# Performance work log

Hardware: AMD Instinct MI355X
Metric: run time of the kernel (lower is better)

## Reference

```python
import jax, jax.numpy as jnp
import numpy as np

B, S, D, H, FB, K, FC = 16, 512, 256, 8, 128, 64, 32


def setup_inputs() -> dict:
    key = jax.random.key(0)
    ks = jax.random.split(key, 16)
    g = lambda i, shp: jax.random.normal(ks[i], shp, dtype=jnp.float32)
    inp = {
        "B_target": g(0, (B, S, FB)),
        "B_infected": g(1, (B, S, FB)),
        "E_target": g(2, (B, S, D)),
        "E_infected": g(3, (B, S, D)),
        "C_target": jax.random.uniform(ks[4], (B, S, K, FC), dtype=jnp.float32),
        "C_infected": jax.random.uniform(ks[5], (B, S, K, FC), dtype=jnp.float32),
        # learned parameters
        "W_bs": g(6, (FB, 1)) * 0.1,
        "W_cs": g(7, (FC, 1)) * 0.1,
        "W1": g(8, (H, D, D)) * (1.0 / np.sqrt(D)),  # per-head Attn W1, batched
        "W2": g(9, (H, D, D)) * (1.0 / np.sqrt(D)),
        "gamma_bs": jnp.ones((S,), jnp.float32),
        "beta_bs": jnp.zeros((S,), jnp.float32),
        "gamma_cs": jnp.ones((S,), jnp.float32),
        "beta_cs": jnp.zeros((S,), jnp.float32),
        "W_f": g(10, (2, 1)) * 0.1,
    }
    return inp


def _weighted_sum(x, W):
    # tf.nn.softmax over trailing size-1 axis of [F,1] -> all ones (faithful)
    return jnp.squeeze(x @ jax.nn.softmax(W, axis=-1), -1)


def _l2norm(x):
    return x * jax.lax.rsqrt(jnp.maximum(jnp.sum(x * x, -1, keepdims=True), 1e-12))


def _layernorm(x, gamma, beta, eps=1e-16):
    m = jnp.mean(x, -1, keepdims=True)
    v = jnp.mean(jnp.square(x - m), -1, keepdims=True)
    return (x - m) * jax.lax.rsqrt(v + eps) * gamma + beta


def _kld(y_true, y_pred, eps=1e-7):
    yt = jnp.clip(y_true, eps, 1.0)
    yp = jnp.clip(y_pred, eps, 1.0)
    return jnp.sum(yt * jnp.log(yt / yp), -1)


def _attn_br(Bvec, E, W1, W2):
    # batched multi-head version of the per-head Attn loop
    Q = jnp.einsum('bsd,hde->bhse', E, W1)
    Kh = jnp.einsum('bsd,hde->bhse', E, W2)
    scale = 1.0 / jnp.sqrt(jnp.asarray(E.shape[-1], E.dtype))
    scores = jnp.einsum('bhse,bhte->bhst', Q, Kh) * scale  # [b,H,S,S]
    A = jax.nn.softmax(scores, axis=2)  # original softmax(axis=1) on [b,S,S]
    # Dot(axes=(1,1)) of [b,S] with [b,S,S] -> [b,S]; stack heads, transpose -> [b,S,H]
    return jnp.einsum('bs,bhst->bth', Bvec, A)


def reference(B_target, B_infected, E_target, E_infected, C_target, C_infected,
              W_bs, W_cs, W1, W2, gamma_bs, beta_bs, gamma_cs, beta_cs, W_f):
    Bt = _weighted_sum(B_target, W_bs)   # [b,S]
    Bi = _weighted_sum(B_infected, W_bs)
    BR_t = _attn_br(Bt, E_target, W1, W2)    # [b,S,H]
    BR_i = _attn_br(Bi, E_infected, W1, W2)
    # keras CosineSimilarity loss = -cos_sim
    cos = -jnp.sum(_l2norm(BR_i) * _l2norm(BR_t), -1)  # [b,S]
    BS_out = _layernorm(cos, gamma_bs, beta_bs)
    Ct = _weighted_sum(C_target, W_cs)   # [b,S,K]
    Ci = _weighted_sum(C_infected, W_cs)
    Cm = 0.5 * (Ct + Ci)
    Cv = 0.5 * _kld(Ci, Cm) + 0.5 * _kld(Ct, Cm)  # [b,S]
    CS_out = _layernorm(Cv, gamma_cs, beta_cs)
    composite = jnp.stack([BS_out, CS_out], axis=-1)  # [b,S,2]
    out = jnp.squeeze(composite @ jax.nn.softmax(W_f, axis=-1), -1)
    return (out, BS_out, CS_out)
```

## Files before the change

### kernel.cpp

```cpp
#include <hip/hip_runtime.h>

#define NB 16
#define NS 512
#define ND 256
#define NH 8
#define NFB 128
#define NK 64
#define NFC 32

using f16 = _Float16;
using f16x4 = __attribute__((ext_vector_type(4))) f16;
using f16x8 = __attribute__((ext_vector_type(8))) f16;
using f32x4 = __attribute__((ext_vector_type(4))) float;

__device__ inline float waveReduceSum(float v) {
    #pragma unroll
    for (int off = 32; off; off >>= 1) v += __shfl_down(v, off);
    return v;
}

__device__ inline f32x4 mfma16(f16x8 a, f16x8 b, f32x4 c) {
    return __builtin_amdgcn_mfma_f32_16x16x32_f16(a, b, c, 0, 0, 0);
}

__global__ __launch_bounds__(256) void k_prep(const float* __restrict__ W1, const float* __restrict__ W2,
                                              f16* __restrict__ Mth,
                                              const float* __restrict__ Et_in, const float* __restrict__ Ei_in,
                                              f16* __restrict__ Ot, f16* __restrict__ Oi,
                                              const float* __restrict__ Bt_in, const float* __restrict__ Bi_in,
                                              float* __restrict__ Bt, float* __restrict__ Bi,
                                              const float* __restrict__ Ct, const float* __restrict__ Ci,
                                              float* __restrict__ Cv) {
    __shared__ float Wa[64][36];
    __shared__ float Wb[64][36];
    int bid = blockIdx.x;
    int tid = threadIdx.x;

    if (bid < 128) {
        int h  = bid >> 4;
        int j0 = ((bid >> 2) & 3) * 64;
        int i0 = (bid & 3) * 64;
        const float* A  = W2 + (size_t)h * ND * ND;
        const float* Bm = W1 + (size_t)h * ND * ND;
        int r = tid >> 4, c = tid & 15;
        float acc[4][4] = {};
        for (int d0 = 0; d0 < ND; d0 += 32) {
            __syncthreads();
            #pragma unroll
            for (int i = 0; i < 2; ++i) {
                int sid = tid + i * 256;
                int row = sid >> 3, seg = sid & 7;
                *(float4*)&Wa[row][seg * 4] = *(const float4*)&A [(size_t)(j0 + row) * ND + d0 + seg * 4];
                *(float4*)&Wb[row][seg * 4] = *(const float4*)&Bm[(size_t)(i0 + row) * ND + d0 + seg * 4];
            }
            __syncthreads();
            #pragma unroll 8
            for (int d = 0; d < 32; ++d) {
                float a0 = Wa[r*4+0][d], a1 = Wa[r*4+1][d], a2 = Wa[r*4+2][d], a3 = Wa[r*4+3][d];
                float b0 = Wb[c*4+0][d], b1 = Wb[c*4+1][d], b2 = Wb[c*4+2][d], b3 = Wb[c*4+3][d];
                acc[0][0] += a0*b0; acc[0][1] += a0*b1; acc[0][2] += a0*b2; acc[0][3] += a0*b3;
                acc[1][0] += a1*b0; acc[1][1] += a1*b1; acc[1][2] += a1*b2; acc[1][3] += a1*b3;
                acc[2][0] += a2*b0; acc[2][1] += a2*b1; acc[2][2] += a2*b2; acc[2][3] += a2*b3;
                acc[3][0] += a3*b0; acc[3][1] += a3*b1; acc[3][2] += a3*b2; acc[3][3] += a3*b3;
            }
        }
        #pragma unroll
        for (int a = 0; a < 4; ++a)
            #pragma unroll
            for (int bb = 0; bb < 4; ++bb)
                Mth[(size_t)h * ND * ND + (size_t)(j0 + r * 4 + a) * ND + (i0 + c * 4 + bb)] = (f16)acc[a][bb];
    } else if (bid < 128 + 4096) {
        const int n4 = NB * NS * ND / 4;
        int i = (bid - 128) * 256 + tid;
        const float* src; f16* dst;
        if (i < n4) { src = Et_in; dst = Ot; }
        else        { src = Ei_in; dst = Oi; i -= n4; }
        float4 v = ((const float4*)src)[i];
        f16x4 o = { (f16)v.x, (f16)v.y, (f16)v.z, (f16)v.w };
        ((f16x4*)dst)[i] = o;
    } else if (bid < 128 + 8192) {
        int wid = ((bid - 128 - 4096) * 256 + tid) >> 6;
        int lane = tid & 63;
        const float* src; float* dst; int row;
        if (wid < NB * NS) { src = Bt_in; dst = Bt; row = wid; }
        else               { src = Bi_in; dst = Bi; row = wid - NB * NS; }
        float2 v = ((const float2*)(src + (size_t)row * NFB))[lane];
        float s = waveReduceSum(v.x + v.y);
        if (lane == 0) dst[row] = s;
    } else {
        int gw = ((bid - 128 - 8192) * 256 + tid) >> 6;
        int lane = tid & 63;
        const float* pt = Ct + ((size_t)gw * NK + lane) * NFC;
        const float* pi = Ci + ((size_t)gw * NK + lane) * NFC;
        float st = 0.f, si = 0.f;
        #pragma unroll
        for (int j = 0; j < NFC; j += 4) {
            float4 vt = *(const float4*)(pt + j); st += vt.x + vt.y + vt.z + vt.w;
            float4 vi = *(const float4*)(pi + j); si += vi.x + vi.y + vi.z + vi.w;
        }
        float cm = 0.5f * (st + si);
        float yp = fminf(fmaxf(cm, 1e-7f), 1.0f);
        float y1 = fminf(fmaxf(si, 1e-7f), 1.0f);
        float y2 = fminf(fmaxf(st, 1e-7f), 1.0f);
        float term = 0.5f * (y1 * logf(y1 / yp) + y2 * logf(y2 / yp));
        term = waveReduceSum(term);
        if (lane == 0) Cv[gw] = term;
    }
}

__global__ __launch_bounds__(256, 4) void k_attn4(const f16* __restrict__ Eft, const f16* __restrict__ Efi,
                                                  const f16* __restrict__ Mth,
                                                  const float* __restrict__ Bst, const float* __restrict__ Bsi,
                                                  float* __restrict__ PEt, float* __restrict__ PBt,
                                                  float* __restrict__ PEi, float* __restrict__ PBi) {
    int x = blockIdx.x;
    const f16* E; const float* Bvg; float *PE, *PB;
    if (x < 512) { E = Eft; Bvg = Bst; PE = PEt; PB = PBt; }
    else         { x -= 512; E = Efi; Bvg = Bsi; PE = PEi; PB = PBi; }
    int b = x >> 5, h = (x >> 2) & 7;
    int sc = x & 3;
    int s0 = sc * 128;
    const f16* Ebase = E + (size_t)b * NS * ND;
    const f16* Mh = Mth + (size_t)h * ND * ND;
    float* PEo = PE + (size_t)((b * NH + h) * 4 + sc) * NS;
    float* PBo = PB + (size_t)((b * NH + h) * 4 + sc) * NS;

    __shared__ f16 smem[2 * 32 * 264];
    __shared__ float pe_s[NS], pb_s[NS];

    int tid = threadIdx.x;
    int lane = tid & 63, w = tid >> 6;
    int l16 = lane & 15, ch = lane >> 4;

    pe_s[tid] = 0.f; pe_s[tid + 256] = 0.f;
    pb_s[tid] = 0.f; pb_s[tid + 256] = 0.f;

    int sw0 = s0 + w * 32;

    f16x8 ebf[2][8];
    #pragma unroll
    for (int st = 0; st < 2; ++st)
        #pragma unroll
        for (int ki = 0; ki < 8; ++ki)
            ebf[st][ki] = *(const f16x8*)&Ebase[(size_t)(sw0 + st * 16 + l16) * ND + ki * 32 + ch * 8];

    float bvr[2][4];
    #pragma unroll
    for (int st = 0; st < 2; ++st)
        #pragma unroll
        for (int r = 0; r < 4; ++r)
            bvr[st][r] = Bvg[b * NS + sw0 + st * 16 + 4 * ch + r];

    f16x8 af[2][8];
    #pragma unroll
    for (int jc = 0; jc < 8; ++jc) {
        __syncthreads();
        #pragma unroll
        for (int it = 0; it < 4; ++it) {
            int sid = tid + it * 256;
            int row = sid >> 5, seg = sid & 31;
            *(int4*)&smem[row * 264 + seg * 8] = *(const int4*)&Mh[(size_t)(jc * 32 + row) * ND + seg * 8];
        }
        __syncthreads();
        f32x4 acc[2][2] = {};
        #pragma unroll
        for (int ki = 0; ki < 8; ++ki) {
            f16x8 a0 = *(const f16x8*)&smem[(l16)      * 264 + ki * 32 + ch * 8];
            f16x8 a1 = *(const f16x8*)&smem[(16 + l16) * 264 + ki * 32 + ch * 8];
            acc[0][0] = mfma16(a0, ebf[0][ki], acc[0][0]);
            acc[0][1] = mfma16(a0, ebf[1][ki], acc[0][1]);
            acc[1][0] = mfma16(a1, ebf[0][ki], acc[1][0]);
            acc[1][1] = mfma16(a1, ebf[1][ki], acc[1][1]);
        }
        #pragma unroll
        for (int st = 0; st < 2; ++st) {
            f16x8 v;
            #pragma unroll
            for (int r = 0; r < 4; ++r) { v[r] = (f16)acc[0][st][r]; v[4 + r] = (f16)acc[1][st][r]; }
            af[st][jc] = v;
        }
    }
    __syncthreads();

    int4 v[4];
    #pragma unroll
    for (int i = 0; i < 4; ++i) {
        int sid = tid + i * 256;
        int row = sid >> 5, seg = sid & 31;
        v[i] = *(const int4*)&Ebase[(size_t)row * ND + seg * 8];
    }
    #pragma unroll
    for (int i = 0; i < 4; ++i) {
        int sid = tid + i * 256;
        int row = sid >> 5, seg = sid & 31;
        *(int4*)&smem[row * 264 + seg * 8] = v[i];
    }

    for (int t = 0; t < 16; ++t) {
        f16* cur = smem + (t & 1) * (32 * 264);
        f16* nxt = smem + ((t + 1) & 1) * (32 * 264);
        if (t < 15) {
            int t0n = (t + 1) * 32;
            #pragma unroll
            for (int i = 0; i < 4; ++i) {
                int sid = tid + i * 256;
                int row = sid >> 5, seg = sid & 31;
                v[i] = *(const int4*)&Ebase[(size_t)(t0n + row) * ND + seg * 8];
            }
        }
        __syncthreads();
        int t0 = t * 32;
        f32x4 sacc[2][2] = {};
        #pragma unroll
        for (int kk = 0; kk < 8; ++kk)
            #pragma unroll
            for (int nt = 0; nt < 2; ++nt) {
                const f16* ep = &cur[(nt * 16 + l16) * 264 + kk * 32 + 4 * ch];
                f16x4 lo = *(const f16x4*)ep;
                f16x4 hi = *(const f16x4*)(ep + 16);
                f16x8 bf = { lo[0], lo[1], lo[2], lo[3], hi[0], hi[1], hi[2], hi[3] };
                sacc[0][nt] = mfma16(af[0][kk], bf, sacc[0][nt]);
                sacc[1][nt] = mfma16(af[1][kk], bf, sacc[1][nt]);
            }
        if (t < 15) {
            #pragma unroll
            for (int i = 0; i < 4; ++i) {
                int sid = tid + i * 256;
                int row = sid >> 5, seg = sid & 31;
                *(int4*)&nxt[row * 264 + seg * 8] = v[i];
            }
        }
        #pragma unroll
        for (int nt = 0; nt < 2; ++nt) {
            float se = 0.f, sw = 0.f;
            #pragma unroll
            for (int st = 0; st < 2; ++st)
                #pragma unroll
                for (int r = 0; r < 4; ++r) {
                    float e = __expf(sacc[st][nt][r] * 0.0625f);
                    se += e; sw += bvr[st][r] * e;
                }
            se += __shfl_down(se, 32); se += __shfl_down(se, 16);
            sw += __shfl_down(sw, 32); sw += __shfl_down(sw, 16);
            if (ch == 0) {
                atomicAdd(&pe_s[t0 + nt * 16 + l16], se);
                atomicAdd(&pb_s[t0 + nt * 16 + l16], sw);
            }
        }
    }
    __syncthreads();
    PEo[tid]       = pe_s[tid];
    PEo[tid + 256] = pe_s[tid + 256];
    PBo[tid]       = pb_s[tid];
    PBo[tid + 256] = pb_s[tid + 256];
}

__global__ __launch_bounds__(512) void k_cos(const float* __restrict__ PEt, const float* __restrict__ PBt,
                                             const float* __restrict__ PEi, const float* __restrict__ PBi,
                                             float* __restrict__ TV, float* __restrict__ IV) {
    int bh = blockIdx.x;
    int s = threadIdx.x;
    float pet = 0.f, pbt = 0.f, pei = 0.f, pbi = 0.f;
    #pragma unroll
    for (int sc = 0; sc < 4; ++sc) {
        size_t idx = (size_t)(bh * 4 + sc) * NS + s;
        pet += PEt[idx]; pbt += PBt[idx];
        pei += PEi[idx]; pbi += PBi[idx];
    }
    TV[(size_t)bh * NS + s] = pbt / pet;
    IV[(size_t)bh * NS + s] = pbi / pei;
}

__device__ inline float blockSum512(float v, float* rbuf) {
    v = waveReduceSum(v);
    int lane = threadIdx.x & 63, w = threadIdx.x >> 6;
    __syncthreads();
    if (lane == 0) rbuf[w] = v;
    __syncthreads();
    float s = 0.f;
    #pragma unroll
    for (int i = 0; i < 8; ++i) s += rbuf[i];
    return s;
}

__global__ __launch_bounds__(512) void k_final(const float* __restrict__ TV, const float* __restrict__ IV,
                                               const float* __restrict__ Cv,
                                               const float* __restrict__ gbs, const float* __restrict__ bbs,
                                               const float* __restrict__ gcs, const float* __restrict__ bcs,
                                               float* __restrict__ out) {
    __shared__ float rbuf[8];
    int b = blockIdx.x, s = threadIdx.x;
    float dot = 0.f, nt = 0.f, nu = 0.f;
    #pragma unroll
    for (int h = 0; h < NH; ++h) {
        float tv = TV[(size_t)(b * NH + h) * NS + s];
        float iv = IV[(size_t)(b * NH + h) * NS + s];
        dot += tv * iv; nt += tv * tv; nu += iv * iv;
    }
    float cosv = -(dot * rsqrtf(fmaxf(nt, 1e-12f)) * rsqrtf(fmaxf(nu, 1e-12f)));

    float mc = blockSum512(cosv, rbuf) * (1.f / 512.f);
    float dc = cosv - mc;
    float vc = blockSum512(dc * dc, rbuf) * (1.f / 512.f);
    float BS = dc * rsqrtf(vc + 1e-16f) * gbs[s] + bbs[s];

    float cv = Cv[(size_t)b * NS + s];
    float mv = blockSum512(cv, rbuf) * (1.f / 512.f);
    float dv = cv - mv;
    float vv = blockSum512(dv * dv, rbuf) * (1.f / 512.f);
    float CS = dv * rsqrtf(vv + 1e-16f) * gcs[s] + bcs[s];

    out[(size_t)b * NS + s] = BS + CS;
    out[(size_t)NB * NS + (size_t)b * NS + s] = BS;
    out[(size_t)2 * NB * NS + (size_t)b * NS + s] = CS;
}

extern "C" void kernel_launch(void* const* d_in, const int* in_sizes, int n_in,
                              void* d_out, int out_size, void* d_ws, size_t ws_size,
                              hipStream_t stream) {
    const float* B_target   = (const float*)d_in[0];
    const float* B_infected = (const float*)d_in[1];
    const float* E_target   = (const float*)d_in[2];
    const float* E_infected = (const float*)d_in[3];
    const float* C_target   = (const float*)d_in[4];
    const float* C_infected = (const float*)d_in[5];
    const float* W1  = (const float*)d_in[8];
    const float* W2  = (const float*)d_in[9];
    const float* gbs = (const float*)d_in[10];
    const float* bbs = (const float*)d_in[11];
    const float* gcs = (const float*)d_in[12];
    const float* bcs = (const float*)d_in[13];
    float* out = (float*)d_out;

    char* ws = (char*)d_ws;
    size_t off = 0;
    auto alloc = [&](size_t n) { char* p = ws + off; off = (off + n + 255) & ~(size_t)255; return p; };
    float* Bt  = (float*)alloc((size_t)NB * NS * 4);
    float* Bi  = (float*)alloc((size_t)NB * NS * 4);
    float* Cv  = (float*)alloc((size_t)NB * NS * 4);
    float* PEt = (float*)alloc((size_t)NB * NH * 4 * NS * 4);
    float* PBt = (float*)alloc((size_t)NB * NH * 4 * NS * 4);
    float* PEi = (float*)alloc((size_t)NB * NH * 4 * NS * 4);
    float* PBi = (float*)alloc((size_t)NB * NH * 4 * NS * 4);
    float* TV  = (float*)alloc((size_t)NB * NH * NS * 4);
    float* IV  = (float*)alloc((size_t)NB * NH * NS * 4);
    f16* Mth = (f16*)alloc((size_t)NH * ND * ND * 2);
    f16* Eft = (f16*)alloc((size_t)NB * NS * ND * 2);
    f16* Efi = (f16*)alloc((size_t)NB * NS * ND * 2);

    k_prep<<<128 + 8192 + 2048, 256, 0, stream>>>(W1, W2, Mth,
                                                  E_target, E_infected, Eft, Efi,
                                                  B_target, B_infected, Bt, Bi,
                                                  C_target, C_infected, Cv);
    k_attn4<<<1024, 256, 0, stream>>>(Eft, Efi, Mth, Bt, Bi, PEt, PBt, PEi, PBi);
    k_cos<<<NB * NH, 512, 0, stream>>>(PEt, PBt, PEi, PBi, TV, IV);
    k_final<<<NB, 512, 0, stream>>>(TV, IV, Cv, gbs, bbs, gcs, bcs, out);
}
```

Before: 339.5 us.

## Read attention operands directly from global memory instead of LDS staging

Removes the shared-memory staging of the per-head M matrix and the double-buffered E tiles in the attention kernel. Each wave now loads its MFMA operands straight from global memory, relying on L1/L2 caching, and most block barriers go away. Launch bounds are relaxed from 4 to 2 blocks per CU to give the compiler more registers. The risk is redundant, poorly coalesced global loads (small 8-byte reads of E) and lower occupancy.

```diff
diff --git a/kernel.cpp b/kernel.cpp
--- a/kernel.cpp
+++ b/kernel.cpp
@@ -108,7 +108,7 @@
     }
 }
 
-__global__ __launch_bounds__(256, 4) void k_attn4(const f16* __restrict__ Eft, const f16* __restrict__ Efi,
+__global__ __launch_bounds__(256, 2) void k_attn4(const f16* __restrict__ Eft, const f16* __restrict__ Efi,
                                                   const f16* __restrict__ Mth,
                                                   const float* __restrict__ Bst, const float* __restrict__ Bsi,
                                                   float* __restrict__ PEt, float* __restrict__ PBt,
@@ -125,7 +125,6 @@
     float* PEo = PE + (size_t)((b * NH + h) * 4 + sc) * NS;
     float* PBo = PB + (size_t)((b * NH + h) * 4 + sc) * NS;
 
-    __shared__ f16 smem[2 * 32 * 264];
     __shared__ float pe_s[NS], pb_s[NS];
 
     int tid = threadIdx.x;
@@ -134,6 +133,7 @@
 
     pe_s[tid] = 0.f; pe_s[tid + 256] = 0.f;
     pb_s[tid] = 0.f; pb_s[tid + 256] = 0.f;
+    __syncthreads();
 
     int sw0 = s0 + w * 32;
 
@@ -154,19 +154,11 @@
     f16x8 af[2][8];
     #pragma unroll
     for (int jc = 0; jc < 8; ++jc) {
-        __syncthreads();
-        #pragma unroll
-        for (int it = 0; it < 4; ++it) {
-            int sid = tid + it * 256;
-            int row = sid >> 5, seg = sid & 31;
-            *(int4*)&smem[row * 264 + seg * 8] = *(const int4*)&Mh[(size_t)(jc * 32 + row) * ND + seg * 8];
-        }
-        __syncthreads();
         f32x4 acc[2][2] = {};
         #pragma unroll
         for (int ki = 0; ki < 8; ++ki) {
-            f16x8 a0 = *(const f16x8*)&smem[(l16)      * 264 + ki * 32 + ch * 8];
-            f16x8 a1 = *(const f16x8*)&smem[(16 + l16) * 264 + ki * 32 + ch * 8];
+            f16x8 a0 = *(const f16x8*)&Mh[(size_t)(jc * 32 + l16)      * ND + ki * 32 + ch * 8];
+            f16x8 a1 = *(const f16x8*)&Mh[(size_t)(jc * 32 + 16 + l16) * ND + ki * 32 + ch * 8];
             acc[0][0] = mfma16(a0, ebf[0][ki], acc[0][0]);
             acc[0][1] = mfma16(a0, ebf[1][ki], acc[0][1]);
             acc[1][0] = mfma16(a1, ebf[0][ki], acc[1][0]);
@@ -180,56 +172,21 @@
             af[st][jc] = v;
         }
     }
-    __syncthreads();
-
-    int4 v[4];
-    #pragma unroll
-    for (int i = 0; i < 4; ++i) {
-        int sid = tid + i * 256;
-        int row = sid >> 5, seg = sid & 31;
-        v[i] = *(const int4*)&Ebase[(size_t)row * ND + seg * 8];
-    }
-    #pragma unroll
-    for (int i = 0; i < 4; ++i) {
-        int sid = tid + i * 256;
-        int row = sid >> 5, seg = sid & 31;
-        *(int4*)&smem[row * 264 + seg * 8] = v[i];
-    }
 
     for (int t = 0; t < 16; ++t) {
-        f16* cur = smem + (t & 1) * (32 * 264);
-        f16* nxt = smem + ((t + 1) & 1) * (32 * 264);
-        if (t < 15) {
-            int t0n = (t + 1) * 32;
-            #pragma unroll
-            for (int i = 0; i < 4; ++i) {
-                int sid = tid + i * 256;
-                int row = sid >> 5, seg = sid & 31;
-                v[i] = *(const int4*)&Ebase[(size_t)(t0n + row) * ND + seg * 8];
-            }
-        }
-        __syncthreads();
         int t0 = t * 32;
         f32x4 sacc[2][2] = {};
         #pragma unroll
         for (int kk = 0; kk < 8; ++kk)
             #pragma unroll
             for (int nt = 0; nt < 2; ++nt) {
-                const f16* ep = &cur[(nt * 16 + l16) * 264 + kk * 32 + 4 * ch];
+                const f16* ep = &Ebase[(size_t)(t0 + nt * 16 + l16) * ND + kk * 32 + 4 * ch];
                 f16x4 lo = *(const f16x4*)ep;
                 f16x4 hi = *(const f16x4*)(ep + 16);
                 f16x8 bf = { lo[0], lo[1], lo[2], lo[3], hi[0], hi[1], hi[2], hi[3] };
                 sacc[0][nt] = mfma16(af[0][kk], bf, sacc[0][nt]);
                 sacc[1][nt] = mfma16(af[1][kk], bf, sacc[1][nt]);
             }
-        if (t < 15) {
-            #pragma unroll
-            for (int i = 0; i < 4; ++i) {
-                int sid = tid + i * 256;
-                int row = sid >> 5, seg = sid & 31;
-                *(int4*)&nxt[row * 264 + seg * 8] = v[i];
-            }
-        }
         #pragma unroll
         for (int nt = 0; nt < 2; ++nt) {
             float se = 0.f, sw = 0.f;
```

Result: slower. 494.8 us (+45.7%).
